# Performance work log

Hardware: AMD Instinct MI355X
Metric: run time of the kernel (lower is better)

The kernel has to match this reference:

```python
import jax, jax.numpy as jnp
import numpy as np

NPOINTS = 1024
RADIUS = 0.2
NSAMPLE = 32


def setup_inputs() -> dict:
    key = jax.random.key(0)
    k1, k2, k3, k4 = jax.random.split(key, 4)
    return {
        "xyz_all": jax.random.uniform(k1, (4, 8192, 3), jnp.float32),
        "normals": jax.random.normal(k2, (4, 8192, 3), jnp.float32),
        "xyz_voxel": jax.random.uniform(k3, (4, 4096, 3), jnp.float32),
        "normals_voxel": jax.random.normal(k4, (4, 4096, 3), jnp.float32),
    }


def _fps(xyz, npoints):
    # Furthest point sampling over a single cloud. xyz: (n, 3) -> (npoints,) int32
    n = xyz.shape[0]

    def body(carry, _):
        dists, last = carry
        d = jnp.sum((xyz - xyz[last]) ** 2, axis=-1)      # (n,) dist^2 to last pick
        dists = jnp.minimum(dists, d)                      # running min dist to set
        nxt = jnp.argmax(dists).astype(jnp.int32)          # farthest point
        return (dists, nxt), nxt

    init = (jnp.full((n,), 1e10, xyz.dtype), jnp.int32(0))
    _, rest = jax.lax.scan(body, init, None, length=npoints - 1)
    return jnp.concatenate([jnp.zeros((1,), jnp.int32), rest])


def _ball_query(xyz, new_xyz, radius, nsample):
    # xyz: (N,3) cloud, new_xyz: (S,3) centers -> (S, nsample) int32 indices
    # squared distances via GEMM form (compute-friendly)
    d2 = (jnp.sum(new_xyz ** 2, -1)[:, None] + jnp.sum(xyz ** 2, -1)[None, :]
          - 2.0 * jnp.einsum('sc,nc->sn', new_xyz, xyz))   # (S, N)
    N = xyz.shape[0]
    cand = jnp.where(d2 < radius * radius, jnp.arange(N, dtype=jnp.int32), N)
    cand = jnp.sort(cand, axis=-1)[:, :nsample]            # first nsample in-ball indices
    first = cand[:, :1]
    idx = jnp.where(cand == N, first, cand)                # pad with first valid index
    return jnp.where(idx == N, 0, idx)                     # degenerate: empty ball -> 0


def reference(xyz_all, normals, xyz_voxel, normals_voxel):
    # FPS on voxel points
    fps_idx = jax.vmap(lambda p: _fps(p, NPOINTS))(xyz_voxel)                 # (B, S)
    new_xyz = jax.vmap(lambda p, i: p[i])(xyz_voxel, fps_idx)                 # (B, S, 3)
    new_normals = jax.vmap(lambda p, i: p[i])(normals_voxel, fps_idx)         # (B, S, 3)
    # Ball query on full cloud
    idx = jax.vmap(lambda p, q: _ball_query(p, q, RADIUS, NSAMPLE))(xyz_all, new_xyz)  # (B, S, ns)
    grouped_xyz = jax.vmap(lambda p, i: p[i])(xyz_all, idx)                   # (B, S, ns, 3)
    rel = grouped_xyz - new_xyz[:, :, None, :]                                # center-relative
    new_features = jnp.transpose(rel, (0, 3, 1, 2))                           # (B, 3, S, ns)
    grouped_n = jax.vmap(lambda f, i: f[i])(normals, idx)                     # (B, S, ns, C)
    new_features_normals = jnp.concatenate(
        [new_features, jnp.transpose(grouped_n, (0, 3, 1, 2))], axis=1)       # (B, 3+C, S, ns)
    return new_xyz, new_normals, new_features, new_features_normals
```

## Files before the change

kernel.cpp:

```cpp
#include <hip/hip_runtime.h>
#include <hip/hip_bf16.h>

#define B 4
#define N_ALL 8192
#define N_VOX 4096
#define S_PTS 1024
#define K_SAMPLE 32
#define R2 0.04f

#define FPS_T 256
#define NPAIR 8
#define PREP_BLOCKS ((B * N_ALL) / FPS_T)

typedef float vf2 __attribute__((ext_vector_type(2)));

__device__ __forceinline__ double mk_key(float v, unsigned int ilo) {
    return __longlong_as_double(
        ((unsigned long long)__float_as_uint(v) << 32) | ilo);
}

__device__ __forceinline__ double wave_key_max_f64(double k) {
    unsigned long long ku = __double_as_longlong(k);
#define DPP_RED(ctrl)                                                              \
    {                                                                              \
        unsigned int lo = (unsigned int)ku;                                        \
        unsigned int hi = (unsigned int)(ku >> 32);                                \
        unsigned int nlo =                                                         \
            (unsigned int)__builtin_amdgcn_update_dpp(0, (int)lo, ctrl, 0xf, 0xf, false); \
        unsigned int nhi =                                                         \
            (unsigned int)__builtin_amdgcn_update_dpp(0, (int)hi, ctrl, 0xf, 0xf, false); \
        double nk = __longlong_as_double(((unsigned long long)nhi << 32) | nlo);   \
        double cur = fmax(__longlong_as_double(ku), nk);                           \
        ku = __double_as_longlong(cur);                                            \
    }
    DPP_RED(0x111);
    DPP_RED(0x112);
    DPP_RED(0x114);
    DPP_RED(0x118);
    DPP_RED(0x142);
    DPP_RED(0x143);
#undef DPP_RED
    return __longlong_as_double(ku);
}

__global__ __launch_bounds__(FPS_T, 1) void fps_prep_kernel(
    const float* __restrict__ xyz_voxel,
    const float* __restrict__ normals_voxel,
    const float* __restrict__ xyz_all,
    float* __restrict__ out_xyz,
    float* __restrict__ out_normals,
    float4* __restrict__ ws_packed,
    int do_prep)
{
#pragma clang fp contract(off)
    if (blockIdx.x >= B) {
        if (!do_prep) return;
        int pid = (blockIdx.x - B) * FPS_T + threadIdx.x;
        if (pid < B * N_ALL) {
            float x = xyz_all[pid * 3 + 0];
            float y = xyz_all[pid * 3 + 1];
            float z = xyz_all[pid * 3 + 2];
            float pp = __fadd_rn(__fadd_rn(__fmul_rn(x, x), __fmul_rn(y, y)),
                                 __fmul_rn(z, z));
            ws_packed[pid] = make_float4(x, y, z, pp);
        }
        return;
    }

    const int b = blockIdx.x;
    const int t = threadIdx.x;
    const int wid = t >> 6;
    const int lane = t & 63;

    __shared__ float4 sp[N_VOX];
    __shared__ int fps_idx_s[S_PTS];
    __shared__ alignas(16) unsigned long long s_part[2][FPS_T / 64];

    const float* xyz = xyz_voxel + (size_t)b * N_VOX * 3;
    for (int i = t; i < N_VOX; i += FPS_T) {
        float x = xyz[i * 3 + 0];
        float y = xyz[i * 3 + 1];
        float z = xyz[i * 3 + 2];
        sp[i] = make_float4(x, y, z, 0.0f);
    }
    __syncthreads();

    vf2 px2[NPAIR], py2[NPAIR], pz2[NPAIR], dist2[NPAIR];
    unsigned int ilo[2 * NPAIR];
#pragma unroll
    for (int jp = 0; jp < NPAIR; jp++) {
        float4 a = sp[t + (2 * jp) * FPS_T];
        float4 c = sp[t + (2 * jp + 1) * FPS_T];
        px2[jp] = vf2{a.x, c.x};
        py2[jp] = vf2{a.y, c.y};
        pz2[jp] = vf2{a.z, c.z};
        dist2[jp] = vf2{1e10f, 1e10f};
        ilo[2 * jp]     = ~(unsigned int)((2 * jp) * FPS_T + t);
        ilo[2 * jp + 1] = ~(unsigned int)((2 * jp + 1) * FPS_T + t);
    }

    if (t == 0) fps_idx_s[0] = 0;
    float4 c0 = sp[0];
    float lx = c0.x, ly = c0.y, lz = c0.z;

    for (int step = 1; step < S_PTS; step++) {
        double kk[2 * NPAIR];
#pragma unroll
        for (int jp = 0; jp < NPAIR; jp++) {
            vf2 dx = px2[jp] - lx;
            vf2 dy = py2[jp] - ly;
            vf2 dz = pz2[jp] - lz;
            vf2 d = (dx * dx + dy * dy) + dz * dz;
            vf2 dm = dist2[jp];
            dm.x = fminf(dm.x, d.x);
            dm.y = fminf(dm.y, d.y);
            dist2[jp] = dm;
            kk[2 * jp]     = mk_key(dm.x, ilo[2 * jp]);
            kk[2 * jp + 1] = mk_key(dm.y, ilo[2 * jp + 1]);
        }
        double m0 = fmax(fmax(kk[0], kk[1]),   fmax(kk[2], kk[3]));
        double m1 = fmax(fmax(kk[4], kk[5]),   fmax(kk[6], kk[7]));
        double m2 = fmax(fmax(kk[8], kk[9]),   fmax(kk[10], kk[11]));
        double m3 = fmax(fmax(kk[12], kk[13]), fmax(kk[14], kk[15]));
        double a0 = fmax(fmax(m0, m1), fmax(m2, m3));
        a0 = wave_key_max_f64(a0);

        const int buf = step & 1;
        if (lane == 63)
            s_part[buf][wid] = (unsigned long long)__double_as_longlong(a0);
        __syncthreads();
        double2 q0 = *((const double2*)&s_part[buf][0]);
        double2 q1 = *((const double2*)&s_part[buf][2]);
        double p0 = fmax(fmax(q0.x, q0.y), fmax(q1.x, q1.y));
        int besti = (int)(~(unsigned int)(unsigned long long)__double_as_longlong(p0))
                    & (N_VOX - 1);
        float4 cb = sp[besti];
        lx = cb.x; ly = cb.y; lz = cb.z;
        if (t == 0) fps_idx_s[step] = besti;
    }
    __syncthreads();

    for (int i = t; i < S_PTS; i += FPS_T) {
        int idx = fps_idx_s[i];
        int o = (b * S_PTS + i) * 3;
        float4 c = sp[idx];
        out_xyz[o + 0] = c.x;
        out_xyz[o + 1] = c.y;
        out_xyz[o + 2] = c.z;
        const float* nv = normals_voxel + ((size_t)b * N_VOX + idx) * 3;
        out_normals[o + 0] = nv[0];
        out_normals[o + 1] = nv[1];
        out_normals[o + 2] = nv[2];
    }
}

template <bool PACKED>
__global__ __launch_bounds__(256) void ballquery_group_kernel(
    const float* __restrict__ xyz_all,
    const float* __restrict__ normals,
    const float* __restrict__ new_xyz,
    const float4* __restrict__ pw,
    float* __restrict__ out_feat,
    float* __restrict__ out_featn)
{
#pragma clang fp contract(off)
    const int wid = threadIdx.x >> 6;
    const int lane = threadIdx.x & 63;
    const int q = blockIdx.x * 4 + wid;
    const int b = q >> 10;
    const int s = q & 1023;

    const float* xyz = xyz_all + (size_t)b * N_ALL * 3;
    const float* nrm = normals + (size_t)b * N_ALL * 3;
    const float4* pwb = PACKED ? (pw + (size_t)b * N_ALL) : nullptr;

    const float qx = new_xyz[q * 3 + 0];
    const float qy = new_xyz[q * 3 + 1];
    const float qz = new_xyz[q * 3 + 2];
    const float qq = __fadd_rn(__fadd_rn(__fmul_rn(qx, qx), __fmul_rn(qy, qy)),
                               __fmul_rn(qz, qz));

    __shared__ int sidx[4][K_SAMPLE];

    int cnt = 0;
    if (PACKED) {
        for (int g = 0; g < N_ALL / 256 && cnt < K_SAMPLE; g++) {
            int base = g * 256 + lane;
            float4 c0 = pwb[base];
            float4 c1 = pwb[base + 64];
            float4 c2 = pwb[base + 128];
            float4 c3 = pwb[base + 192];
            vf2 pxA = vf2{c0.x, c1.x}, pxB = vf2{c2.x, c3.x};
            vf2 pyA = vf2{c0.y, c1.y}, pyB = vf2{c2.y, c3.y};
            vf2 pzA = vf2{c0.z, c1.z}, pzB = vf2{c2.z, c3.z};
            vf2 ppA = vf2{c0.w, c1.w}, ppB = vf2{c2.w, c3.w};
            vf2 dtA = qx * pxA; dtA = dtA + qy * pyA; dtA = dtA + qz * pzA;
            vf2 dtB = qx * pxB; dtB = dtB + qy * pyB; dtB = dtB + qz * pzB;
            vf2 d2A = (qq + ppA) - 2.0f * dtA;
            vf2 d2B = (qq + ppB) - 2.0f * dtB;
            float d2s[4] = {d2A.x, d2A.y, d2B.x, d2B.y};
#pragma unroll
            for (int u = 0; u < 4; u++) {
                bool hit = d2s[u] < R2;
                unsigned long long mask = __ballot(hit);
                if (hit) {
                    int pos = cnt + __popcll(mask & ((1ull << lane) - 1ull));
                    if (pos < K_SAMPLE) sidx[wid][pos] = g * 256 + u * 64 + lane;
                }
                cnt += (int)__popcll(mask);
            }
        }
    } else {
        for (int c = 0; c < N_ALL / 64 && cnt < K_SAMPLE; c++) {
            int i = c * 64 + lane;
            float px = xyz[i * 3 + 0];
            float py = xyz[i * 3 + 1];
            float pz = xyz[i * 3 + 2];
            float pp = __fadd_rn(__fadd_rn(__fmul_rn(px, px), __fmul_rn(py, py)),
                                 __fmul_rn(pz, pz));
            float dt = __fadd_rn(__fadd_rn(__fmul_rn(qx, px), __fmul_rn(qy, py)),
                                 __fmul_rn(qz, pz));
            float d2 = __fsub_rn(__fadd_rn(qq, pp), __fmul_rn(2.0f, dt));
            bool hit = d2 < R2;
            unsigned long long mask = __ballot(hit);
            if (hit) {
                int pos = cnt + __popcll(mask & ((1ull << lane) - 1ull));
                if (pos < K_SAMPLE) sidx[wid][pos] = i;
            }
            cnt += (int)__popcll(mask);
        }
    }
    __syncthreads();

    if (lane < K_SAMPLE) {
        int idxj;
        if (cnt == 0)        idxj = 0;
        else if (lane < cnt) idxj = sidx[wid][lane];
        else                 idxj = sidx[wid][0];

        float px, py, pz;
        if (PACKED) {
            float4 cc = pwb[idxj];
            px = cc.x; py = cc.y; pz = cc.z;
        } else {
            px = xyz[idxj * 3 + 0];
            py = xyz[idxj * 3 + 1];
            pz = xyz[idxj * 3 + 2];
        }
        float rx = __fsub_rn(px, qx);
        float ry = __fsub_rn(py, qy);
        float rz = __fsub_rn(pz, qz);

        int o3 = ((b * 3) * S_PTS + s) * K_SAMPLE + lane;
        out_feat[o3 + 0 * 32768] = rx;
        out_feat[o3 + 1 * 32768] = ry;
        out_feat[o3 + 2 * 32768] = rz;

        float nx = nrm[idxj * 3 + 0];
        float ny = nrm[idxj * 3 + 1];
        float nz = nrm[idxj * 3 + 2];

        int o4 = ((b * 6) * S_PTS + s) * K_SAMPLE + lane;
        out_featn[o4 + 0 * 32768] = rx;
        out_featn[o4 + 1 * 32768] = ry;
        out_featn[o4 + 2 * 32768] = rz;
        out_featn[o4 + 3 * 32768] = nx;
        out_featn[o4 + 4 * 32768] = ny;
        out_featn[o4 + 5 * 32768] = nz;
    }
}

extern "C" void kernel_launch(void* const* d_in, const int* in_sizes, int n_in,
                              void* d_out, int out_size, void* d_ws, size_t ws_size,
                              hipStream_t stream) {
    const float* xyz_all       = (const float*)d_in[0];
    const float* normals       = (const float*)d_in[1];
    const float* xyz_voxel     = (const float*)d_in[2];
    const float* normals_voxel = (const float*)d_in[3];

    float* out = (float*)d_out;
    float* out_xyz     = out;
    float* out_normals = out + 12288;
    float* out_feat    = out + 24576;
    float* out_featn   = out + 417792;

    const size_t need = (size_t)B * N_ALL * sizeof(float4);
    const bool use_ws = ws_size >= need;

    fps_prep_kernel<<<B + (use_ws ? PREP_BLOCKS : 0), FPS_T, 0, stream>>>(
        xyz_voxel, normals_voxel, xyz_all, out_xyz, out_normals,
        (float4*)d_ws, use_ws ? 1 : 0);

    if (use_ws) {
        ballquery_group_kernel<true><<<(B * S_PTS) / 4, 256, 0, stream>>>(
            xyz_all, normals, out_xyz, (const float4*)d_ws, out_feat, out_featn);
    } else {
        ballquery_group_kernel<false><<<(B * S_PTS) / 4, 256, 0, stream>>>(
            xyz_all, normals, out_xyz, nullptr, out_feat, out_featn);
    }
}
```

Measured before the change: 584.6 us.

## Pack two batch FPS problems into one 512-thread block

Each FPS block now runs two batches, one per half of a 512-thread block, with per-half shared memory copies of points, indices and partial maxima. Only two FPS blocks are launched instead of four, and both halves share one __syncthreads per step. This places two sequential FPS chains on the same CU, which could improve latency hiding for the serial argmax chain. The cost is that each barrier now waits for both halves, and the block uses twice as much LDS (about 140KB).

After: 836.3 us. +43.1%, slower.

```diff
diff --git a/kernel.cpp b/kernel.cpp
--- a/kernel.cpp
+++ b/kernel.cpp
@@ -8,8 +8,10 @@
 #define K_SAMPLE 32
 #define R2 0.04f
 
-#define FPS_T 256
+#define FPS_T 512
+#define HALF_T 256
 #define NPAIR 8
+#define FPS_BLOCKS 2
 #define PREP_BLOCKS ((B * N_ALL) / FPS_T)
 
 typedef float vf2 __attribute__((ext_vector_type(2)));
@@ -53,9 +55,9 @@
     int do_prep)
 {
 #pragma clang fp contract(off)
-    if (blockIdx.x >= B) {
+    if (blockIdx.x >= FPS_BLOCKS) {
         if (!do_prep) return;
-        int pid = (blockIdx.x - B) * FPS_T + threadIdx.x;
+        int pid = (blockIdx.x - FPS_BLOCKS) * FPS_T + threadIdx.x;
         if (pid < B * N_ALL) {
             float x = xyz_all[pid * 3 + 0];
             float y = xyz_all[pid * 3 + 1];
@@ -67,21 +69,23 @@
         return;
     }
 
-    const int b = blockIdx.x;
     const int t = threadIdx.x;
-    const int wid = t >> 6;
+    const int half = t >> 8;
+    const int tl = t & (HALF_T - 1);
+    const int b = blockIdx.x * 2 + half;
+    const int wid = tl >> 6;
     const int lane = t & 63;
 
-    __shared__ float4 sp[N_VOX];
-    __shared__ int fps_idx_s[S_PTS];
-    __shared__ alignas(16) unsigned long long s_part[2][FPS_T / 64];
+    __shared__ float4 sp[2][N_VOX];
+    __shared__ int fps_idx_s[2][S_PTS];
+    __shared__ alignas(16) unsigned long long s_part[2][2][HALF_T / 64];
 
     const float* xyz = xyz_voxel + (size_t)b * N_VOX * 3;
-    for (int i = t; i < N_VOX; i += FPS_T) {
+    for (int i = tl; i < N_VOX; i += HALF_T) {
         float x = xyz[i * 3 + 0];
         float y = xyz[i * 3 + 1];
         float z = xyz[i * 3 + 2];
-        sp[i] = make_float4(x, y, z, 0.0f);
+        sp[half][i] = make_float4(x, y, z, 0.0f);
     }
     __syncthreads();
 
@@ -89,18 +93,18 @@
     unsigned int ilo[2 * NPAIR];
 #pragma unroll
     for (int jp = 0; jp < NPAIR; jp++) {
-        float4 a = sp[t + (2 * jp) * FPS_T];
-        float4 c = sp[t + (2 * jp + 1) * FPS_T];
+        float4 a = sp[half][tl + (2 * jp) * HALF_T];
+        float4 c = sp[half][tl + (2 * jp + 1) * HALF_T];
         px2[jp] = vf2{a.x, c.x};
         py2[jp] = vf2{a.y, c.y};
         pz2[jp] = vf2{a.z, c.z};
         dist2[jp] = vf2{1e10f, 1e10f};
-        ilo[2 * jp]     = ~(unsigned int)((2 * jp) * FPS_T + t);
-        ilo[2 * jp + 1] = ~(unsigned int)((2 * jp + 1) * FPS_T + t);
-    }
-
-    if (t == 0) fps_idx_s[0] = 0;
-    float4 c0 = sp[0];
+        ilo[2 * jp]     = ~(unsigned int)((2 * jp) * HALF_T + tl);
+        ilo[2 * jp + 1] = ~(unsigned int)((2 * jp + 1) * HALF_T + tl);
+    }
+
+    if (tl == 0) fps_idx_s[half][0] = 0;
+    float4 c0 = sp[half][0];
     float lx = c0.x, ly = c0.y, lz = c0.z;
 
     for (int step = 1; step < S_PTS; step++) {
@@ -127,23 +131,23 @@
 
         const int buf = step & 1;
         if (lane == 63)
-            s_part[buf][wid] = (unsigned long long)__double_as_longlong(a0);
+            s_part[half][buf][wid] = (unsigned long long)__double_as_longlong(a0);
         __syncthreads();
-        double2 q0 = *((const double2*)&s_part[buf][0]);
-        double2 q1 = *((const double2*)&s_part[buf][2]);
+        double2 q0 = *((const double2*)&s_part[half][buf][0]);
+        double2 q1 = *((const double2*)&s_part[half][buf][2]);
         double p0 = fmax(fmax(q0.x, q0.y), fmax(q1.x, q1.y));
         int besti = (int)(~(unsigned int)(unsigned long long)__double_as_longlong(p0))
                     & (N_VOX - 1);
-        float4 cb = sp[besti];
+        float4 cb = sp[half][besti];
         lx = cb.x; ly = cb.y; lz = cb.z;
-        if (t == 0) fps_idx_s[step] = besti;
+        if (tl == 0) fps_idx_s[half][step] = besti;
     }
     __syncthreads();
 
-    for (int i = t; i < S_PTS; i += FPS_T) {
-        int idx = fps_idx_s[i];
+    for (int i = tl; i < S_PTS; i += HALF_T) {
+        int idx = fps_idx_s[half][i];
         int o = (b * S_PTS + i) * 3;
-        float4 c = sp[idx];
+        float4 c = sp[half][idx];
         out_xyz[o + 0] = c.x;
         out_xyz[o + 1] = c.y;
         out_xyz[o + 2] = c.z;
@@ -287,7 +291,7 @@
     const size_t need = (size_t)B * N_ALL * sizeof(float4);
     const bool use_ws = ws_size >= need;
 
-    fps_prep_kernel<<<B + (use_ws ? PREP_BLOCKS : 0), FPS_T, 0, stream>>>(
+    fps_prep_kernel<<<FPS_BLOCKS + (use_ws ? PREP_BLOCKS : 0), FPS_T, 0, stream>>>(
         xyz_voxel, normals_voxel, xyz_all, out_xyz, out_normals,
         (float4*)d_ws, use_ws ? 1 : 0);
 
```
